# Kernel optimization log

Hardware: AMD Instinct MI355X
Metric: run time of the kernel (lower is better)

The kernel has to match this reference:

```python
import jax, jax.numpy as jnp
import numpy as np

B, S, E, F = 8, 1024, 1024, 4096
EPS = 1e-12

def _layer_norm(x, gamma, beta):
    mu = jnp.mean(x, axis=-1, keepdims=True)
    var = jnp.mean(jnp.square(x - mu), axis=-1, keepdims=True)
    return (x - mu) / jnp.sqrt(var + EPS) * gamma + beta

def setup_inputs() -> dict:
    key = jax.random.key(0)
    ks = jax.random.split(key, 16)
    sE = 1.0 / np.sqrt(E)
    sF = 1.0 / np.sqrt(F)
    return {
        'hidden_states': jax.random.normal(ks[0], (B, S, E), jnp.float32),
        'Wq': jax.random.normal(ks[1], (E, E), jnp.float32) * sE,
        'bq': jnp.zeros((E,), jnp.float32),
        'Wk': jax.random.normal(ks[2], (E, E), jnp.float32) * sE,
        'bk': jnp.zeros((E,), jnp.float32),
        'Wv': jax.random.normal(ks[3], (E, E), jnp.float32) * sE,
        'bv': jnp.zeros((E,), jnp.float32),
        'Wd': jax.random.normal(ks[4], (E, E), jnp.float32) * sE,
        'bd': jnp.zeros((E,), jnp.float32),
        'g1': jnp.ones((E,), jnp.float32),
        'b1': jnp.zeros((E,), jnp.float32),
        'Wi': jax.random.normal(ks[5], (E, F), jnp.float32) * sE,
        'bi': jnp.zeros((F,), jnp.float32),
        'Wo': jax.random.normal(ks[6], (F, E), jnp.float32) * sF,
        'bo': jnp.zeros((E,), jnp.float32),
        'g2': jnp.ones((E,), jnp.float32),
        'b2': jnp.zeros((E,), jnp.float32),
    }

def reference(hidden_states, Wq, bq, Wk, bk, Wv, bv, Wd, bd, g1, b1, Wi, bi, Wo, bo, g2, b2):
    x = hidden_states
    q = x @ Wq + bq                     # [B,S,E]
    k = x @ Wk + bk
    v = x @ Wv + bv
    scores = jnp.einsum('bqe,bke->bqk', q, k) / jnp.sqrt(jnp.float32(E))
    attn_w = jax.nn.softmax(scores, axis=-1)
    attn_out = jnp.einsum('bqk,bke->bqe', attn_w, v)
    # add_norm 1 (dropout = identity in eval)
    h1 = _layer_norm(attn_out @ Wd + bd + x, g1, b1)
    ff = jax.nn.gelu(h1 @ Wi + bi, approximate=False)   # forward_act
    # NOTE: original code's second add_norm uses forward_act (pre out_dense),
    # applying out_dense inside add_norm -> LN(out_dense(ff) + h1)
    out = _layer_norm(ff @ Wo + bo + h1, g2, b2)
    return out
```

## Files before the change

kernel.cpp:

```cpp
#include <hip/hip_runtime.h>
#include <math.h>


typedef __bf16 bf16;
typedef __attribute__((ext_vector_type(8))) __bf16 bf16x8;
typedef __attribute__((ext_vector_type(4))) __bf16 bf16x4;
typedef __attribute__((ext_vector_type(4))) float f32x4;

#define BM 128
#define BN 128
#define BK 64
#define SCS 140

__device__ __forceinline__ void async_cp16(const bf16* g, bf16* l) {
    __builtin_amdgcn_global_load_lds((__attribute__((address_space(1))) void*)(g),
                                     (__attribute__((address_space(3))) void*)(l),
                                     16, 0, 0);
}

__device__ __forceinline__ float gelu_fast(float x) {
    float u = x * x;
    float y = 1.5957691216f * x * fmaf(0.044715f, u, 1.0f);
    float e = __expf(-y);
    return x * __builtin_amdgcn_rcpf(1.0f + e);
}

__device__ __forceinline__ float load_dual(const void* p, long long i, int f32) {
    return f32 ? ((const float*)p)[i] : (float)((const bf16*)p)[i];
}


__global__ void diag_init(const void* x, int* dflag)
{
    const int t = threadIdx.x;
    const bf16* xb = (const bf16*)x;
    float a = (float)xb[2 * t];
    float b = (float)xb[2 * t + 1];
    auto wild = [](float v) -> bool {
        float af = fabsf(v);
        return !(af <= 3.0e38f) || af > 1.0e3f || (v != 0.0f && af < 1.0e-8f);
    };
    unsigned long long ba = __ballot(wild(a));
    unsigned long long bb = __ballot(wild(b));
    if (t == 0) *dflag = (__popcll(ba) + __popcll(bb) > 16) ? 1 : 0;
}

__global__ void sentinel_small(float* out) { out[0] = 2048.0f; }


__global__ __launch_bounds__(256)
void convert_vec4(const void* src, bf16* dst, long long n4, const int* dflag)
{
    const int f32 = *dflag;
    long long i = (long long)blockIdx.x * 256 + threadIdx.x;
    if (i >= n4) return;
    bf16x4 o;
    if (f32) {
        f32x4 v = ((const f32x4*)src)[i];
        #pragma unroll
        for (int j = 0; j < 4; j++) o[j] = (bf16)v[j];
    } else {
        o = ((const bf16x4*)src)[i];
    }
    ((bf16x4*)dst)[i] = o;
}

struct SmallPtrs { const void* p[10]; };

__global__ __launch_bounds__(256)
void convert_small(SmallPtrs sp, bf16* dst, const int* dflag)
{
    const int f32 = *dflag;
    const int idx = blockIdx.x * 256 + threadIdx.x;
    if (idx >= 13312) return;
    const int seg = idx >> 10;
    float v;
    if (seg < 9) v = load_dual(sp.p[seg], idx & 1023, f32);
    else         v = load_dual(sp.p[9], idx - 9216, f32);
    dst[idx] = (bf16)v;
}

__global__ __launch_bounds__(256)
void transpose_dual(const void* in, bf16* out, int R, int C, const int* dflag)
{
    __shared__ bf16 tile[32][33];
    const int f32 = *dflag;
    const int c0 = blockIdx.x * 32, r0 = blockIdx.y * 32;
    const int tx = threadIdx.x, ty = threadIdx.y;
    #pragma unroll
    for (int i = 0; i < 32; i += 8)
        tile[ty + i][tx] = (bf16)load_dual(in, (long long)(r0 + ty + i) * C + (c0 + tx), f32);
    __syncthreads();
    #pragma unroll
    for (int i = 0; i < 32; i += 8)
        out[(long long)(c0 + ty + i) * R + (r0 + tx)] = tile[tx][ty + i];
}

__global__ __launch_bounds__(256)
void transpose_b(const bf16* __restrict__ in, bf16* __restrict__ out, int R, int C)
{
    __shared__ bf16 tile[32][33];
    const long long z = (long long)blockIdx.z * (long long)R * C;
    const int c0 = blockIdx.x * 32, r0 = blockIdx.y * 32;
    const int tx = threadIdx.x, ty = threadIdx.y;
    #pragma unroll
    for (int i = 0; i < 32; i += 8)
        tile[ty + i][tx] = in[z + (long long)(r0 + ty + i) * C + (c0 + tx)];
    __syncthreads();
    #pragma unroll
    for (int i = 0; i < 32; i += 8)
        out[z + (long long)(c0 + ty + i) * R + (r0 + tx)] = tile[tx][ty + i];
}

template<int ACT, int HAS_BIAS, int HAS_RES, int OUT_F32>
__global__ __launch_bounds__(256)
void gemm_bt(const bf16* __restrict__ A, const bf16* __restrict__ Bt,
             const bf16* __restrict__ bias, const bf16* __restrict__ res,
             void* __restrict__ Cout, int M, int N, int K, float scale,
             long long bsA, long long bsB, long long bsC, long long bsBias)
{
    __shared__ __align__(16) char smem[SCS * 64 * 4];
    bf16* sA = (bf16*)smem;
    bf16* sB = (bf16*)(smem + 16384);
    float* sC = (float*)smem;

    const int tid  = threadIdx.x;
    const int lane = tid & 63;
    const int wave = tid >> 6;
    const int wm   = wave >> 1;
    const int wn   = wave & 1;
    const int m0   = blockIdx.y * BM;
    const int n0   = blockIdx.x * BN;
    const long long zA = (long long)blockIdx.z * bsA;
    const long long zB = (long long)blockIdx.z * bsB;
    const long long zC = (long long)blockIdx.z * bsC;
    const bf16* biasz = HAS_BIAS ? (bias + (long long)blockIdx.z * bsBias) : nullptr;

    const bf16* gA[4]; const bf16* gB[4];
    bf16* lA[4]; bf16* lB[4];
    #pragma unroll
    for (int j = 0; j < 4; j++) {
        const int ci  = j * 256 + tid;
        const int row = ci >> 3;
        const int c8  = ((ci & 7) ^ (row & 7)) * 8;
        gA[j] = A + zA + (long long)(m0 + row) * K + c8;
        gB[j] = Bt + zB + (long long)(n0 + row) * K + c8;
        lA[j] = sA + (j * 256 + wave * 64) * 8;
        lB[j] = sB + (j * 256 + wave * 64) * 8;
    }

    f32x4 acc[4][4];
    const f32x4 zf = {0.f, 0.f, 0.f, 0.f};
    #pragma unroll
    for (int i = 0; i < 4; i++)
        #pragma unroll
        for (int j = 0; j < 4; j++) acc[i][j] = zf;

    const int fr   = lane & 15;
    const int x0   = (lane >> 4) ^ (fr & 7);
    const int arow = wm * 64 + fr;
    const int brow = wn * 64 + fr;

    for (int kt = 0; kt < K; kt += BK) {
        #pragma unroll
        for (int j = 0; j < 4; j++) {
            async_cp16(gA[j], lA[j]);
            async_cp16(gB[j], lB[j]);
            gA[j] += BK; gB[j] += BK;
        }
        __syncthreads();

        #pragma unroll
        for (int s = 0; s < 2; s++) {
            const int xo = (x0 ^ (s << 2)) * 8;
            bf16x8 afr[4], bfr[4];
            #pragma unroll
            for (int mi = 0; mi < 4; mi++) afr[mi] = *(const bf16x8*)(sA + (arow + mi * 16) * 64 + xo);
            #pragma unroll
            for (int ni = 0; ni < 4; ni++) bfr[ni] = *(const bf16x8*)(sB + (brow + ni * 16) * 64 + xo);
            #pragma unroll
            for (int mi = 0; mi < 4; mi++)
                #pragma unroll
                for (int ni = 0; ni < 4; ni++)
                    acc[mi][ni] = __builtin_amdgcn_mfma_f32_16x16x32_bf16(afr[mi], bfr[ni], acc[mi][ni], 0, 0, 0);
        }
        __syncthreads();
    }

    const int q4 = lane >> 4;
    for (int h = 0; h < 2; h++) {
        __syncthreads();
        if (wm == h) {
            #pragma unroll
            for (int mi = 0; mi < 4; mi++)
                #pragma unroll
                for (int r = 0; r < 4; r++) {
                    const int lr = mi * 16 + q4 * 4 + r;
                    #pragma unroll
                    for (int ni = 0; ni < 4; ni++)
                        sC[lr * SCS + wn * 64 + ni * 16 + fr] = acc[mi][ni][r];
                }
        }
        __syncthreads();
        const int lr = tid >> 2;
        const int cb = (tid & 3) * 32;
        const long long grow  = m0 + h * 64 + lr;
        const long long gbase = zC + grow * (long long)N + (n0 + cb);
        const float* srow = sC + lr * SCS + cb;
        #pragma unroll
        for (int k8 = 0; k8 < 4; k8++) {
            f32x4 v0 = *(const f32x4*)(srow + k8 * 8);
            f32x4 v1 = *(const f32x4*)(srow + k8 * 8 + 4);
            float vv[8] = {v0[0], v0[1], v0[2], v0[3], v1[0], v1[1], v1[2], v1[3]};
            if constexpr (HAS_BIAS) {
                bf16x8 bb = *(const bf16x8*)(biasz + n0 + cb + k8 * 8);
                #pragma unroll
                for (int j = 0; j < 8; j++) vv[j] = vv[j] * scale + (float)bb[j];
            } else {
                #pragma unroll
                for (int j = 0; j < 8; j++) vv[j] *= scale;
            }
            if constexpr (ACT == 1) {
                #pragma unroll
                for (int j = 0; j < 8; j++) vv[j] = gelu_fast(vv[j]);
            }
            if constexpr (HAS_RES) {
                bf16x8 rr = *(const bf16x8*)(res + gbase + k8 * 8);
                #pragma unroll
                for (int j = 0; j < 8; j++) vv[j] += (float)rr[j];
            }
            if constexpr (OUT_F32) {
                f32x4 o0 = {vv[0], vv[1], vv[2], vv[3]};
                f32x4 o1 = {vv[4], vv[5], vv[6], vv[7]};
                *(f32x4*)((float*)Cout + gbase + k8 * 8)     = o0;
                *(f32x4*)((float*)Cout + gbase + k8 * 8 + 4) = o1;
            } else {
                bf16x8 o;
                #pragma unroll
                for (int j = 0; j < 8; j++) o[j] = (bf16)vv[j];
                *(bf16x8*)((bf16*)Cout + gbase + k8 * 8) = o;
            }
        }
    }
}


__global__ __launch_bounds__(256)
void softmax_inplace(bf16* __restrict__ P, int N)
{
    const long long row = blockIdx.x;
    bf16* p = P + row * (long long)N;
    const int t = threadIdx.x;
    bf16x4 xin = *(const bf16x4*)(p + t * 4);
    float xs[4];
    #pragma unroll
    for (int i = 0; i < 4; i++) xs[i] = (float)xin[i];

    float m = fmaxf(fmaxf(xs[0], xs[1]), fmaxf(xs[2], xs[3]));
    #pragma unroll
    for (int off = 32; off > 0; off >>= 1) m = fmaxf(m, __shfl_xor(m, off, 64));
    __shared__ float red[4];
    if ((t & 63) == 0) red[t >> 6] = m;
    __syncthreads();
    m = fmaxf(fmaxf(red[0], red[1]), fmaxf(red[2], red[3]));

    float e[4], s = 0.f;
    #pragma unroll
    for (int i = 0; i < 4; i++) { e[i] = __expf(xs[i] - m); s += e[i]; }
    #pragma unroll
    for (int off = 32; off > 0; off >>= 1) s += __shfl_xor(s, off, 64);
    __shared__ float red2[4];
    if ((t & 63) == 0) red2[t >> 6] = s;
    __syncthreads();
    s = red2[0] + red2[1] + red2[2] + red2[3];
    const float inv = 1.f / s;

    bf16x4 o;
    #pragma unroll
    for (int i = 0; i < 4; i++) o[i] = (bf16)(e[i] * inv);
    *(bf16x4*)(p + t * 4) = o;
}

template<int IN_F32, int OUT_F32>
__global__ __launch_bounds__(256)
void layernorm_rows(const void* __restrict__ Z, const bf16* __restrict__ g,
                    const bf16* __restrict__ b, void* __restrict__ outp, int N)
{
    const long long row = blockIdx.x;
    const int t = threadIdx.x;
    float xv[4];
    if constexpr (IN_F32) {
        f32x4 zin = *(const f32x4*)((const float*)Z + row * (long long)N + t * 4);
        #pragma unroll
        for (int i = 0; i < 4; i++) xv[i] = zin[i];
    } else {
        bf16x4 zin = *(const bf16x4*)((const bf16*)Z + row * (long long)N + t * 4);
        #pragma unroll
        for (int i = 0; i < 4; i++) xv[i] = (float)zin[i];
    }

    float s = xv[0] + xv[1] + xv[2] + xv[3];
    #pragma unroll
    for (int off = 32; off > 0; off >>= 1) s += __shfl_xor(s, off, 64);
    __shared__ float r1[4];
    if ((t & 63) == 0) r1[t >> 6] = s;
    __syncthreads();
    const float mu = (r1[0] + r1[1] + r1[2] + r1[3]) * (1.f / 1024.f);

    float d[4];
    float sq = 0.f;
    #pragma unroll
    for (int i = 0; i < 4; i++) { d[i] = xv[i] - mu; sq += d[i] * d[i]; }
    #pragma unroll
    for (int off = 32; off > 0; off >>= 1) sq += __shfl_xor(sq, off, 64);
    __shared__ float r2[4];
    if ((t & 63) == 0) r2[t >> 6] = sq;
    __syncthreads();
    const float var = (r2[0] + r2[1] + r2[2] + r2[3]) * (1.f / 1024.f);
    const float rstd = rsqrtf(var + 1e-12f);

    bf16x4 gv = *(const bf16x4*)(g + t * 4);
    bf16x4 bv = *(const bf16x4*)(b + t * 4);
    if constexpr (OUT_F32) {
        f32x4 o;
        #pragma unroll
        for (int i = 0; i < 4; i++)
            o[i] = d[i] * rstd * (float)gv[i] + (float)bv[i];
        *(f32x4*)((float*)outp + row * (long long)N + t * 4) = o;
    } else {
        bf16x4 o;
        #pragma unroll
        for (int i = 0; i < 4; i++)
            o[i] = (bf16)(d[i] * rstd * (float)gv[i] + (float)bv[i]);
        *(bf16x4*)((bf16*)outp + row * (long long)N + t * 4) = o;
    }
}


extern "C" void kernel_launch(void* const* d_in, const int* in_sizes, int n_in,
                              void* d_out, int out_size, void* d_ws, size_t ws_size,
                              hipStream_t stream)
{
    (void)in_sizes; (void)n_in; (void)out_size;

    const void* x  = d_in[0];
    const void* Wq = d_in[1];  const void* bq = d_in[2];
    const void* Wk = d_in[3];  const void* bk = d_in[4];
    const void* Wv = d_in[5];  const void* bv = d_in[6];
    const void* Wd = d_in[7];  const void* bd = d_in[8];
    const void* g1 = d_in[9];  const void* b1 = d_in[10];
    const void* Wi = d_in[11]; const void* bi = d_in[12];
    const void* Wo = d_in[13]; const void* bo = d_in[14];
    const void* g2 = d_in[15]; const void* b2 = d_in[16];

    const int Bb = 8, S = 1024, E = 1024, F = 4096;
    const int M = Bb * S;
    const long long SE = (long long)S * E, SS = (long long)S * S;
    const long long ME = (long long)M * E;

    char* ws = (char*)d_ws;
    const size_t MB = 1024ull * 1024ull;
    int*  dflag = (int*)(ws + 0);
    bf16* small = (bf16*)(ws + 64 * 1024);
    bf16* bq_c = small + 0 * 1024;
    bf16* bd_c = small + 3 * 1024;
    bf16* g1_c = small + 4 * 1024;
    bf16* b1_c = small + 5 * 1024;
    bf16* g2_c = small + 6 * 1024;
    bf16* b2_c = small + 7 * 1024;
    bf16* bo_c = small + 8 * 1024;
    bf16* bi_c = small + 9216;
    bf16* WoT  = (bf16*)(ws + 1 * MB);
    bf16* WiT  = (bf16*)(ws + 9 * MB);
    bf16* WqT  = (bf16*)(ws + 17 * MB);
    bf16* WkT  = (bf16*)(ws + 19 * MB);
    bf16* WvT  = (bf16*)(ws + 21 * MB);
    bf16* WdT  = (bf16*)(ws + 23 * MB);
    bf16* xb   = (bf16*)(ws + 25 * MB);
    float* out = (float*)d_out;

    diag_init<<<1, 64, 0, stream>>>(x, dflag);

    if (ws_size < 70 * MB) { sentinel_small<<<1, 1, 0, stream>>>(out); return; }

    SmallPtrs sp;
    sp.p[0] = bq; sp.p[1] = bk; sp.p[2] = bv; sp.p[3] = bd; sp.p[4] = g1;
    sp.p[5] = b1; sp.p[6] = g2; sp.p[7] = b2; sp.p[8] = bo; sp.p[9] = bi;
    convert_small<<<52, 256, 0, stream>>>(sp, small, dflag);
    convert_vec4<<<8192, 256, 0, stream>>>(x, xb, ME / 4, dflag);

    const dim3 tb(32, 8, 1);
    transpose_dual<<<dim3(E/32, E/32), tb, 0, stream>>>(Wq, WqT, E, E, dflag);
    transpose_dual<<<dim3(E/32, E/32), tb, 0, stream>>>(Wk, WkT, E, E, dflag);
    transpose_dual<<<dim3(E/32, E/32), tb, 0, stream>>>(Wv, WvT, E, E, dflag);
    transpose_dual<<<dim3(E/32, E/32), tb, 0, stream>>>(Wd, WdT, E, E, dflag);
    transpose_dual<<<dim3(F/32, E/32), tb, 0, stream>>>(Wi, WiT, E, F, dflag);
    transpose_dual<<<dim3(E/32, F/32), tb, 0, stream>>>(Wo, WoT, F, E, dflag);

    if (ws_size >= 121 * MB) {
        bf16* qkv  = (bf16*)(ws + 41 * MB);
        bf16* q    = qkv;
        bf16* k    = qkv + ME;
        bf16* v    = qkv + 2 * ME;
        bf16* vT   = (bf16*)(ws + 89 * MB);
        bf16* P    = (bf16*)(ws + 73 * MB);
        bf16* attn = (bf16*)(ws + 41 * MB);
        bf16* z1   = (bf16*)(ws + 57 * MB);
        bf16* h1   = (bf16*)(ws + 41 * MB);
        bf16* ff   = (bf16*)(ws + 57 * MB);
        float* z2f = (float*)(ws + 9 * MB);

        gemm_bt<0,1,0,0><<<dim3(8, 64, 3), 256, 0, stream>>>(
            xb, WqT, bq_c, nullptr, qkv, M, E, E, 1.f, 0, (long long)E * E, ME, E);
        transpose_b<<<dim3(E/32, S/32, Bb), tb, 0, stream>>>(v, vT, S, E);
        gemm_bt<0,0,0,0><<<dim3(8, 8, Bb), 256, 0, stream>>>(
            q, k, nullptr, nullptr, P, S, S, E, 0.03125f, SE, SE, SS, 0);
        softmax_inplace<<<M, 256, 0, stream>>>(P, S);
        gemm_bt<0,0,0,0><<<dim3(8, 8, Bb), 256, 0, stream>>>(
            P, vT, nullptr, nullptr, attn, S, E, S, 1.f, SS, SE, SE, 0);
        gemm_bt<0,1,1,0><<<dim3(8, 64), 256, 0, stream>>>(
            attn, WdT, bd_c, xb, z1, M, E, E, 1.f, 0, 0, 0, 0);
        layernorm_rows<0,0><<<M, 256, 0, stream>>>(z1, g1_c, b1_c, h1, E);
        gemm_bt<1,1,0,0><<<dim3(32, 64), 256, 0, stream>>>(
            h1, WiT, bi_c, nullptr, ff, M, F, E, 1.f, 0, 0, 0, 0);
        gemm_bt<0,1,1,1><<<dim3(8, 64), 256, 0, stream>>>(
            ff, WoT, bo_c, h1, z2f, M, E, F, 1.f, 0, 0, 0, 0);
        layernorm_rows<1,1><<<M, 256, 0, stream>>>(z2f, g2_c, b2_c, out, E);
    } else {
        bf16* qkv_b = (bf16*)(ws + 41 * MB);
        bf16* q_b   = qkv_b;
        bf16* k_b   = qkv_b + SE;
        bf16* v_b   = qkv_b + 2 * SE;
        bf16* vT_b  = (bf16*)(ws + 47 * MB);
        bf16* P_b   = (bf16*)(ws + 49 * MB);
        bf16* at_b  = (bf16*)(ws + 51 * MB);
        bf16* z1_b  = (bf16*)(ws + 53 * MB);
        bf16* h1_b  = (bf16*)(ws + 55 * MB);
        bf16* ff_b  = (bf16*)(ws + 57 * MB);
        bf16* z2_b  = (bf16*)(ws + 65 * MB);

        for (int b = 0; b < Bb; b++) {
            const bf16* x_b = xb + (long long)b * SE;
            gemm_bt<0,1,0,0><<<dim3(8, 8, 3), 256, 0, stream>>>(
                x_b, WqT, bq_c, nullptr, qkv_b, S, E, E, 1.f, 0, (long long)E * E, SE, E);
            transpose_b<<<dim3(E/32, S/32), tb, 0, stream>>>(v_b, vT_b, S, E);
            gemm_bt<0,0,0,0><<<dim3(8, 8), 256, 0, stream>>>(
                q_b, k_b, nullptr, nullptr, P_b, S, S, E, 0.03125f, 0, 0, 0, 0);
            softmax_inplace<<<S, 256, 0, stream>>>(P_b, S);
            gemm_bt<0,0,0,0><<<dim3(8, 8), 256, 0, stream>>>(
                P_b, vT_b, nullptr, nullptr, at_b, S, E, S, 1.f, 0, 0, 0, 0);
            gemm_bt<0,1,1,0><<<dim3(8, 8), 256, 0, stream>>>(
                at_b, WdT, bd_c, x_b, z1_b, S, E, E, 1.f, 0, 0, 0, 0);
            layernorm_rows<0,0><<<S, 256, 0, stream>>>(z1_b, g1_c, b1_c, h1_b, E);
            gemm_bt<1,1,0,0><<<dim3(32, 8), 256, 0, stream>>>(
                h1_b, WiT, bi_c, nullptr, ff_b, S, F, E, 1.f, 0, 0, 0, 0);
            gemm_bt<0,1,1,0><<<dim3(8, 8), 256, 0, stream>>>(
                ff_b, WoT, bo_c, h1_b, z2_b, S, E, F, 1.f, 0, 0, 0, 0);
            layernorm_rows<0,1><<<S, 256, 0, stream>>>(z2_b, g2_c, b2_c, out + (long long)b * SE, E);
        }
    }
}
```

Baseline: 573.1 us.

## Warp-specialize GEMM with producer waves and double-buffered LDS

Splits each GEMM block into four producer waves that issue async global-to-LDS copies and four consumer waves that run MFMA. LDS is double-buffered so the next K tile loads while the current one is computed, removing one barrier per iteration. Block size doubles to 512 threads and LDS use rises to 64KB, which cuts resident blocks per CU and leaves half the waves idle for math.

```diff
diff --git a/kernel.cpp b/kernel.cpp
--- a/kernel.cpp
+++ b/kernel.cpp
@@ -113,76 +113,96 @@
 }
 
 template<int ACT, int HAS_BIAS, int HAS_RES, int OUT_F32>
-__global__ __launch_bounds__(256)
+__global__ __launch_bounds__(512)
 void gemm_bt(const bf16* __restrict__ A, const bf16* __restrict__ Bt,
              const bf16* __restrict__ bias, const bf16* __restrict__ res,
              void* __restrict__ Cout, int M, int N, int K, float scale,
              long long bsA, long long bsB, long long bsC, long long bsBias)
 {
-    __shared__ __align__(16) char smem[SCS * 64 * 4];
-    bf16* sA = (bf16*)smem;
-    bf16* sB = (bf16*)(smem + 16384);
+    __shared__ __align__(16) char smem[65536];
     float* sC = (float*)smem;
 
     const int tid  = threadIdx.x;
     const int lane = tid & 63;
     const int wave = tid >> 6;
-    const int wm   = wave >> 1;
-    const int wn   = wave & 1;
+    const int pw   = wave & 3;
+    const int wm   = pw >> 1;
+    const int wn   = pw & 1;
+    const bool producer = (wave >= 4);
     const int m0   = blockIdx.y * BM;
     const int n0   = blockIdx.x * BN;
     const long long zA = (long long)blockIdx.z * bsA;
     const long long zB = (long long)blockIdx.z * bsB;
     const long long zC = (long long)blockIdx.z * bsC;
     const bf16* biasz = HAS_BIAS ? (bias + (long long)blockIdx.z * bsBias) : nullptr;
-
-    const bf16* gA[4]; const bf16* gB[4];
-    bf16* lA[4]; bf16* lB[4];
-    #pragma unroll
-    for (int j = 0; j < 4; j++) {
-        const int ci  = j * 256 + tid;
-        const int row = ci >> 3;
-        const int c8  = ((ci & 7) ^ (row & 7)) * 8;
-        gA[j] = A + zA + (long long)(m0 + row) * K + c8;
-        gB[j] = Bt + zB + (long long)(n0 + row) * K + c8;
-        lA[j] = sA + (j * 256 + wave * 64) * 8;
-        lB[j] = sB + (j * 256 + wave * 64) * 8;
-    }
+    const int nIter = K >> 6;
 
     f32x4 acc[4][4];
-    const f32x4 zf = {0.f, 0.f, 0.f, 0.f};
-    #pragma unroll
-    for (int i = 0; i < 4; i++)
-        #pragma unroll
-        for (int j = 0; j < 4; j++) acc[i][j] = zf;
+    const bf16* gA[4]; const bf16* gB[4]; int lo[4];
+
+    if (producer) {
+        #pragma unroll
+        for (int j = 0; j < 4; j++) {
+            const int ci  = j * 256 + pw * 64 + lane;
+            const int row = ci >> 3;
+            const int c8  = ((ci & 7) ^ (row & 7)) * 8;
+            gA[j] = A + zA + (long long)(m0 + row) * K + c8;
+            gB[j] = Bt + zB + (long long)(n0 + row) * K + c8;
+            lo[j] = (j * 256 + pw * 64) * 8;
+        }
+        bf16* dA = (bf16*)smem;
+        bf16* dB = (bf16*)(smem + 16384);
+        #pragma unroll
+        for (int j = 0; j < 4; j++) {
+            async_cp16(gA[j], dA + lo[j]);
+            async_cp16(gB[j], dB + lo[j]);
+            gA[j] += BK; gB[j] += BK;
+        }
+    } else {
+        const f32x4 zf = {0.f, 0.f, 0.f, 0.f};
+        #pragma unroll
+        for (int i = 0; i < 4; i++)
+            #pragma unroll
+            for (int j = 0; j < 4; j++) acc[i][j] = zf;
+    }
+    __syncthreads();
 
     const int fr   = lane & 15;
     const int x0   = (lane >> 4) ^ (fr & 7);
     const int arow = wm * 64 + fr;
     const int brow = wn * 64 + fr;
 
-    for (int kt = 0; kt < K; kt += BK) {
-        #pragma unroll
-        for (int j = 0; j < 4; j++) {
-            async_cp16(gA[j], lA[j]);
-            async_cp16(gB[j], lB[j]);
-            gA[j] += BK; gB[j] += BK;
-        }
-        __syncthreads();
-
-        #pragma unroll
-        for (int s = 0; s < 2; s++) {
-            const int xo = (x0 ^ (s << 2)) * 8;
-            bf16x8 afr[4], bfr[4];
+    for (int kt = 0; kt < nIter; ++kt) {
+        if (producer) {
+            if (kt + 1 < nIter) {
+                const int bo = ((kt + 1) & 1) ? 32768 : 0;
+                bf16* dA = (bf16*)(smem + bo);
+                bf16* dB = (bf16*)(smem + bo + 16384);
+                #pragma unroll
+                for (int j = 0; j < 4; j++) {
+                    async_cp16(gA[j], dA + lo[j]);
+                    async_cp16(gB[j], dB + lo[j]);
+                    gA[j] += BK; gB[j] += BK;
+                }
+            }
+        } else {
+            const int bo = (kt & 1) ? 32768 : 0;
+            const bf16* sAk = (const bf16*)(smem + bo);
+            const bf16* sBk = (const bf16*)(smem + bo + 16384);
             #pragma unroll
-            for (int mi = 0; mi < 4; mi++) afr[mi] = *(const bf16x8*)(sA + (arow + mi * 16) * 64 + xo);
-            #pragma unroll
-            for (int ni = 0; ni < 4; ni++) bfr[ni] = *(const bf16x8*)(sB + (brow + ni * 16) * 64 + xo);
-            #pragma unroll
-            for (int mi = 0; mi < 4; mi++)
-                #pragma unroll
-                for (int ni = 0; ni < 4; ni++)
-                    acc[mi][ni] = __builtin_amdgcn_mfma_f32_16x16x32_bf16(afr[mi], bfr[ni], acc[mi][ni], 0, 0, 0);
+            for (int s = 0; s < 2; s++) {
+                const int xo = (x0 ^ (s << 2)) * 8;
+                bf16x8 afr[4], bfr[4];
+                #pragma unroll
+                for (int mi = 0; mi < 4; mi++) afr[mi] = *(const bf16x8*)(sAk + (arow + mi * 16) * 64 + xo);
+                #pragma unroll
+                for (int ni = 0; ni < 4; ni++) bfr[ni] = *(const bf16x8*)(sBk + (brow + ni * 16) * 64 + xo);
+                #pragma unroll
+                for (int mi = 0; mi < 4; mi++)
+                    #pragma unroll
+                    for (int ni = 0; ni < 4; ni++)
+                        acc[mi][ni] = __builtin_amdgcn_mfma_f32_16x16x32_bf16(afr[mi], bfr[ni], acc[mi][ni], 0, 0, 0);
+            }
         }
         __syncthreads();
     }
@@ -190,7 +210,7 @@
     const int q4 = lane >> 4;
     for (int h = 0; h < 2; h++) {
         __syncthreads();
-        if (wm == h) {
+        if (!producer && wm == h) {
             #pragma unroll
             for (int mi = 0; mi < 4; mi++)
                 #pragma unroll
@@ -202,18 +222,18 @@
                 }
         }
         __syncthreads();
-        const int lr = tid >> 2;
-        const int cb = (tid & 3) * 32;
+        const int lr = tid >> 3;
+        const int cb = (tid & 7) * 16;
         const long long grow  = m0 + h * 64 + lr;
         const long long gbase = zC + grow * (long long)N + (n0 + cb);
         const float* srow = sC + lr * SCS + cb;
         #pragma unroll
-        for (int k8 = 0; k8 < 4; k8++) {
-            f32x4 v0 = *(const f32x4*)(srow + k8 * 8);
-            f32x4 v1 = *(const f32x4*)(srow + k8 * 8 + 4);
+        for (int g = 0; g < 2; g++) {
+            f32x4 v0 = *(const f32x4*)(srow + g * 8);
+            f32x4 v1 = *(const f32x4*)(srow + g * 8 + 4);
             float vv[8] = {v0[0], v0[1], v0[2], v0[3], v1[0], v1[1], v1[2], v1[3]};
             if constexpr (HAS_BIAS) {
-                bf16x8 bb = *(const bf16x8*)(biasz + n0 + cb + k8 * 8);
+                bf16x8 bb = *(const bf16x8*)(biasz + n0 + cb + g * 8);
                 #pragma unroll
                 for (int j = 0; j < 8; j++) vv[j] = vv[j] * scale + (float)bb[j];
             } else {
@@ -225,20 +245,20 @@
                 for (int j = 0; j < 8; j++) vv[j] = gelu_fast(vv[j]);
             }
             if constexpr (HAS_RES) {
-                bf16x8 rr = *(const bf16x8*)(res + gbase + k8 * 8);
+                bf16x8 rr = *(const bf16x8*)(res + gbase + g * 8);
                 #pragma unroll
                 for (int j = 0; j < 8; j++) vv[j] += (float)rr[j];
             }
             if constexpr (OUT_F32) {
                 f32x4 o0 = {vv[0], vv[1], vv[2], vv[3]};
                 f32x4 o1 = {vv[4], vv[5], vv[6], vv[7]};
-                *(f32x4*)((float*)Cout + gbase + k8 * 8)     = o0;
-                *(f32x4*)((float*)Cout + gbase + k8 * 8 + 4) = o1;
+                *(f32x4*)((float*)Cout + gbase + g * 8)     = o0;
+                *(f32x4*)((float*)Cout + gbase + g * 8 + 4) = o1;
             } else {
                 bf16x8 o;
                 #pragma unroll
                 for (int j = 0; j < 8; j++) o[j] = (bf16)vv[j];
-                *(bf16x8*)((bf16*)Cout + gbase + k8 * 8) = o;
+                *(bf16x8*)((bf16*)Cout + gbase + g * 8) = o;
             }
         }
     }
@@ -410,20 +430,20 @@
         bf16* ff   = (bf16*)(ws + 57 * MB);
         float* z2f = (float*)(ws + 9 * MB);
 
-        gemm_bt<0,1,0,0><<<dim3(8, 64, 3), 256, 0, stream>>>(
+        gemm_bt<0,1,0,0><<<dim3(8, 64, 3), 512, 0, stream>>>(
             xb, WqT, bq_c, nullptr, qkv, M, E, E, 1.f, 0, (long long)E * E, ME, E);
         transpose_b<<<dim3(E/32, S/32, Bb), tb, 0, stream>>>(v, vT, S, E);
-        gemm_bt<0,0,0,0><<<dim3(8, 8, Bb), 256, 0, stream>>>(
+        gemm_bt<0,0,0,0><<<dim3(8, 8, Bb), 512, 0, stream>>>(
             q, k, nullptr, nullptr, P, S, S, E, 0.03125f, SE, SE, SS, 0);
         softmax_inplace<<<M, 256, 0, stream>>>(P, S);
-        gemm_bt<0,0,0,0><<<dim3(8, 8, Bb), 256, 0, stream>>>(
+        gemm_bt<0,0,0,0><<<dim3(8, 8, Bb), 512, 0, stream>>>(
             P, vT, nullptr, nullptr, attn, S, E, S, 1.f, SS, SE, SE, 0);
-        gemm_bt<0,1,1,0><<<dim3(8, 64), 256, 0, stream>>>(
+        gemm_bt<0,1,1,0><<<dim3(8, 64), 512, 0, stream>>>(
             attn, WdT, bd_c, xb, z1, M, E, E, 1.f, 0, 0, 0, 0);
         layernorm_rows<0,0><<<M, 256, 0, stream>>>(z1, g1_c, b1_c, h1, E);
-        gemm_bt<1,1,0,0><<<dim3(32, 64), 256, 0, stream>>>(
+        gemm_bt<1,1,0,0><<<dim3(32, 64), 512, 0, stream>>>(
             h1, WiT, bi_c, nullptr, ff, M, F, E, 1.f, 0, 0, 0, 0);
-        gemm_bt<0,1,1,1><<<dim3(8, 64), 256, 0, stream>>>(
+        gemm_bt<0,1,1,1><<<dim3(8, 64), 512, 0, stream>>>(
             ff, WoT, bo_c, h1, z2f, M, E, F, 1.f, 0, 0, 0, 0);
         layernorm_rows<1,1><<<M, 256, 0, stream>>>(z2f, g2_c, b2_c, out, E);
     } else {
@@ -441,20 +461,20 @@
 
         for (int b = 0; b < Bb; b++) {
             const bf16* x_b = xb + (long long)b * SE;
-            gemm_bt<0,1,0,0><<<dim3(8, 8, 3), 256, 0, stream>>>(
+            gemm_bt<0,1,0,0><<<dim3(8, 8, 3), 512, 0, stream>>>(
                 x_b, WqT, bq_c, nullptr, qkv_b, S, E, E, 1.f, 0, (long long)E * E, SE, E);
             transpose_b<<<dim3(E/32, S/32), tb, 0, stream>>>(v_b, vT_b, S, E);
-            gemm_bt<0,0,0,0><<<dim3(8, 8), 256, 0, stream>>>(
+            gemm_bt<0,0,0,0><<<dim3(8, 8), 512, 0, stream>>>(
                 q_b, k_b, nullptr, nullptr, P_b, S, S, E, 0.03125f, 0, 0, 0, 0);
             softmax_inplace<<<S, 256, 0, stream>>>(P_b, S);
-            gemm_bt<0,0,0,0><<<dim3(8, 8), 256, 0, stream>>>(
+            gemm_bt<0,0,0,0><<<dim3(8, 8), 512, 0, stream>>>(
                 P_b, vT_b, nullptr, nullptr, at_b, S, E, S, 1.f, 0, 0, 0, 0);
-            gemm_bt<0,1,1,0><<<dim3(8, 8), 256, 0, stream>>>(
+            gemm_bt<0,1,1,0><<<dim3(8, 8), 512, 0, stream>>>(
                 at_b, WdT, bd_c, x_b, z1_b, S, E, E, 1.f, 0, 0, 0, 0);
             layernorm_rows<0,0><<<S, 256, 0, stream>>>(z1_b, g1_c, b1_c, h1_b, E);
-            gemm_bt<1,1,0,0><<<dim3(32, 8), 256, 0, stream>>>(
+            gemm_bt<1,1,0,0><<<dim3(32, 8), 512, 0, stream>>>(
                 h1_b, WiT, bi_c, nullptr, ff_b, S, F, E, 1.f, 0, 0, 0, 0);
-            gemm_bt<0,1,1,0><<<dim3(8, 8), 256, 0, stream>>>(
+            gemm_bt<0,1,1,0><<<dim3(8, 8), 512, 0, stream>>>(
                 ff_b, WoT, bo_c, h1_b, z2_b, S, E, F, 1.f, 0, 0, 0, 0);
             layernorm_rows<0,1><<<S, 256, 0, stream>>>(z2_b, g2_c, b2_c, out + (long long)b * SE, E);
         }
```

After: 530.7 us. -7.4%, faster.
